# Performance work log

Measured on AMD Instinct MI355X. Metric: run time of the kernel, lower is better.

## Reference

```python
import jax, jax.numpy as jnp
import numpy as np

B, N, E = 32, 2048, 1048576  # 32 uniform graphs of 2048 nodes, avg degree 16
BN = B * N
KS = (1024, 512, 256)  # TopKPooling ratio=0.5 -> ceil(0.5*n) per layer (uniform graphs -> static)


def _mlp2(x, w1, b1, w2, b2):
    # nn.Sequential(Linear, ReLU, Linear)
    return jnp.maximum(x @ w1 + b1, 0.0) @ w2 + b2


def _forward(x, edge_attr, node_w1, node_b1, node_w2, node_b2,
             edge_w1, edge_b1, edge_w2, edge_b2,
             eff_in_w, eff_in_b, eff_h_w, eff_h_b, eff_out_w, eff_out_b,
             upd_in_w, upd_in_b, upd_h_w, upd_h_b, upd_out_w, upd_out_b,
             pool_w, edge_index):
    relu = lambda t: jnp.maximum(t, 0.0)
    src, dst = edge_index[0], edge_index[1]  # PyG: x_j = h[src], x_i = h[dst], aggregate at dst
    h = _mlp2(x, node_w1, node_b1, node_w2, node_b2)          # [BN, F] node embedding
    e = _mlp2(edge_attr, edge_w1, edge_b1, edge_w2, edge_b2)  # [E, F]  edge embedding
    node_mask = jnp.ones((BN,), bool)
    edge_mask = jnp.ones((E,), bool)
    for i in range(3):
        # --- DPIGNNLayer: gather-concat-MLP(+edge_attr) message, scatter-mean aggregate ---
        m = jnp.concatenate([h[dst], h[src]], axis=-1)        # [E, 2F] = cat(x_i, x_j)
        m = relu(m @ eff_in_w[i] + eff_in_b[i])
        m = relu(m @ eff_h_w[i] + eff_h_b[i])
        m = relu(m @ eff_out_w[i] + eff_out_b[i] + e)
        em = edge_mask.astype(h.dtype)[:, None]
        agg = jax.ops.segment_sum(m * em, dst, num_segments=BN)
        cnt = jax.ops.segment_sum(em, dst, num_segments=BN)
        mean = agg / jnp.maximum(cnt, 1.0)                    # mean aggr (0 where no edges)
        u = jnp.concatenate([mean, h], axis=-1)
        u = relu(u @ upd_in_w[i] + upd_in_b[i])
        u = relu(u @ upd_h_w[i] + upd_h_b[i])
        _ = relu(u @ upd_out_w[i] + upd_out_b[i] + h)  # dead compute: source update() returns x
        # --- TopKPooling(ratio=0.5), masked form (uniform graph sizes -> static k) ---
        w = pool_w[i]
        score = jnp.tanh((h @ w) / jnp.linalg.norm(w))        # [BN]
        masked = jnp.where(node_mask, score, -jnp.inf).reshape(B, N)
        _, idx = jax.lax.top_k(masked, KS[i])                 # [B, k]
        sel = jnp.zeros((B, N), bool).at[jnp.arange(B)[:, None], idx].set(True).reshape(-1)
        node_mask = sel
        h = jnp.where(node_mask[:, None], h * score[:, None], 0.0)
        edge_mask = edge_mask & node_mask[src] & node_mask[dst]  # filter_adj equivalent
    # global_mean_pool over surviving nodes per graph
    nm = node_mask.astype(h.dtype)[:, None]
    sums = (h * nm).reshape(B, N, -1).sum(axis=1)
    cnts = nm.reshape(B, N, 1).sum(axis=1)
    return sums / jnp.maximum(cnts, 1.0)  # [B, F]


def setup_inputs() -> dict:
    key = jax.random.key(0)
    ks = iter(jax.random.split(key, 40))
    F, ND, ED = 128, 16, 8
    s = 0.05
    W = lambda shape: jax.random.normal(next(ks), shape, jnp.float32) * s
    zb = lambda shape: jnp.zeros(shape, jnp.float32)
    e_per = E // B
    base = (jnp.arange(E) // e_per) * N  # graph offset per edge
    src = jax.random.randint(next(ks), (E,), 0, N) + base
    dst = jax.random.randint(next(ks), (E,), 0, N) + base
    return {
        'x': jax.random.normal(next(ks), (BN, ND), jnp.float32),
        'edge_attr': jax.random.normal(next(ks), (E, ED), jnp.float32),
        'node_w1': W((ND, F)), 'node_b1': zb((F,)),
        'node_w2': W((F, F)), 'node_b2': zb((F,)),
        'edge_w1': W((ED, F)), 'edge_b1': zb((F,)),
        'edge_w2': W((F, F)), 'edge_b2': zb((F,)),
        'eff_in_w': W((3, 2 * F, F)), 'eff_in_b': zb((3, F)),
        'eff_h_w': W((3, F, F)), 'eff_h_b': zb((3, F)),
        'eff_out_w': W((3, F, F)), 'eff_out_b': zb((3, F)),
        'upd_in_w': W((3, 2 * F, F)), 'upd_in_b': zb((3, F)),
        'upd_h_w': W((3, F, F)), 'upd_h_b': zb((3, F)),
        'upd_out_w': W((3, F, F)), 'upd_out_b': zb((3, F)),
        'pool_w': W((3, F)),
        'edge_index': jnp.stack([src, dst]),
    }


def reference(x, edge_attr, node_w1, node_b1, node_w2, node_b2,
              edge_w1, edge_b1, edge_w2, edge_b2,
              eff_in_w, eff_in_b, eff_h_w, eff_h_b, eff_out_w, eff_out_b,
              upd_in_w, upd_in_b, upd_h_w, upd_h_b, upd_out_w, upd_out_b,
              pool_w, edge_index):
    return _forward(x, edge_attr, node_w1, node_b1, node_w2, node_b2,
                    edge_w1, edge_b1, edge_w2, edge_b2,
                    eff_in_w, eff_in_b, eff_h_w, eff_h_b, eff_out_w, eff_out_b,
                    upd_in_w, upd_in_b, upd_h_w, upd_h_b, upd_out_w, upd_out_b,
                    pool_w, edge_index)
```

## Files before the change

### kernel.cpp

```cpp
#include <hip/hip_runtime.h>
#include <hip/hip_bf16.h>


#define NPG    2048
#define NGRAPH 32
#define HP     2112
#define HPAD(b) ((b) + ((b) >> 5))

__device__ __forceinline__ unsigned int mono_bits(float z) {
    unsigned int bb = __float_as_uint(z);
    return (bb & 0x80000000u) ? ~bb : (bb | 0x80000000u);
}
__device__ __forceinline__ float mono_decode(unsigned int mo) {
    unsigned int bb = (mo & 0x80000000u) ? (mo & 0x7FFFFFFFu) : ~mo;
    return __uint_as_float(bb);
}

__global__ __launch_bounds__(256) void k1_fused(
    const float* __restrict__ x,
    const float* __restrict__ W1,
    const float* __restrict__ b1,
    const float* __restrict__ W2,
    const float* __restrict__ b2,
    const float* __restrict__ pw,
    float4* __restrict__ d4)
{
    __shared__ __align__(16) float swn[384];
    __shared__ __align__(16) float sv[384];
    __shared__ float sc[4];
    __shared__ float snorm[3];
    int t = threadIdx.x;
    int lane = t & 63, wv = t >> 6;

    if (wv < 3) {
        float w0 = pw[wv * 128 + lane];
        float w1 = pw[wv * 128 + 64 + lane];
        float p = w0 * w0 + w1 * w1;
        #pragma unroll
        for (int s = 32; s; s >>= 1) p += __shfl_xor(p, s);
        if (lane == 0) snorm[wv] = sqrtf(p);
    }
    __syncthreads();
    for (int i = t; i < 384; i += 256) swn[i] = pw[i] / snorm[i >> 7];
    __syncthreads();
    for (int task = t; task < 387; task += 256) {
        int k = task / 129, j = task % 129;
        const float4* r4 = (const float4*)((j < 128) ? (W2 + j * 128) : b2);
        const float* wn = swn + k * 128;
        float p0 = 0.f, p1 = 0.f, p2 = 0.f, p3 = 0.f;
        #pragma unroll 8
        for (int q = 0; q < 32; ++q) {
            float4 w = r4[q];
            p0 = fmaf(w.x, wn[4 * q + 0], p0);
            p1 = fmaf(w.y, wn[4 * q + 1], p1);
            p2 = fmaf(w.z, wn[4 * q + 2], p2);
            p3 = fmaf(w.w, wn[4 * q + 3], p3);
        }
        float p = (p0 + p1) + (p2 + p3);
        if (j < 128) sv[k * 128 + j] = p;
        else sc[k] = p;
    }
    __syncthreads();

    const float4* W1v = (const float4*)W1;
    const float4* b1v = (const float4*)b1;
    int n = blockIdx.x * 256 + t;
    const float4* xr = (const float4*)(x + (size_t)n * 16);
    float4 xa = xr[0], xb = xr[1], xc = xr[2], xd = xr[3];
    float xs[16] = {xa.x, xa.y, xa.z, xa.w, xb.x, xb.y, xb.z, xb.w,
                    xc.x, xc.y, xc.z, xc.w, xd.x, xd.y, xd.z, xd.w};
    const float4* sv4 = (const float4*)sv;
    float dd0 = sc[0], dd1 = sc[1], dd2 = sc[2];
    #pragma unroll 4
    for (int fq = 0; fq < 32; ++fq) {
        float4 a4 = b1v[fq];
        #pragma unroll
        for (int j = 0; j < 16; ++j) {
            float4 w = W1v[j * 32 + fq];
            a4.x = fmaf(xs[j], w.x, a4.x);
            a4.y = fmaf(xs[j], w.y, a4.y);
            a4.z = fmaf(xs[j], w.z, a4.z);
            a4.w = fmaf(xs[j], w.w, a4.w);
        }
        a4.x = fmaxf(a4.x, 0.f); a4.y = fmaxf(a4.y, 0.f);
        a4.z = fmaxf(a4.z, 0.f); a4.w = fmaxf(a4.w, 0.f);
        float4 v0 = sv4[fq], v1 = sv4[32 + fq], v2 = sv4[64 + fq];
        dd0 = fmaf(a4.x, v0.x, fmaf(a4.y, v0.y, fmaf(a4.z, v0.z, fmaf(a4.w, v0.w, dd0))));
        dd1 = fmaf(a4.x, v1.x, fmaf(a4.y, v1.y, fmaf(a4.z, v1.z, fmaf(a4.w, v1.w, dd1))));
        dd2 = fmaf(a4.x, v2.x, fmaf(a4.y, v2.y, fmaf(a4.z, v2.z, fmaf(a4.w, v2.w, dd2))));
    }
    d4[n] = make_float4(dd0, dd1, dd2, 0.f);
}

__global__ __launch_bounds__(1024, 1) void k2_cascade(
    const float* __restrict__ x,
    const float* __restrict__ W1,
    const float* __restrict__ b1,
    const float* __restrict__ W2,
    const float* __restrict__ b2,
    const float4* __restrict__ d4,
    float* __restrict__ out)
{
    __shared__ unsigned long long sKey[NPG];
    __shared__ float d1A[NPG], d2A[NPG];
    __shared__ unsigned int hist[2][HP];
    __shared__ int   idxB[1024];
    __shared__ float cscB[1024], d1B[1024], d2B[1024];
    __shared__ int   idxA2[512];
    __shared__ float cscA2[512], d2A2[512];
    __shared__ float sW1[2048], sb1[128];
    __shared__ float Spart[1024], Svec[128], red4[4];
    __shared__ unsigned long long sPrefix;
    __shared__ int sNeed, sDone, sCnt;

    int t = threadIdx.x, g = blockIdx.x;
    int lane = t & 63, wv = t >> 6;
    const float4* d4g = d4 + (size_t)g * NPG;

    float4 e0 = d4g[t];
    float4 e1 = d4g[t + 1024];
    for (int i = t; i < 2048; i += 1024) sW1[i] = W1[i];
    if (t < 128) sb1[t] = b1[t];
    for (int i = t; i < 2 * HP; i += 1024) ((unsigned int*)hist)[i] = 0u;
    if (t == 0) { sPrefix = 0ull; sNeed = 1024; sDone = 0; sCnt = 0; }
    __syncthreads();

    {
        unsigned long long kv0 = ((unsigned long long)mono_bits(e0.x) << 11)
                               | (unsigned long long)(unsigned int)(2047 - t);
        d1A[t] = e0.y; d2A[t] = e0.z;
        sKey[t] = kv0;
        atomicAdd(&hist[0][HPAD((unsigned int)(kv0 >> 33) & 2047u)], 1u);
        int n1 = t + 1024;
        unsigned long long kv1 = ((unsigned long long)mono_bits(e1.x) << 11)
                               | (unsigned long long)(unsigned int)(2047 - n1);
        d1A[n1] = e1.y; d2A[n1] = e1.z;
        sKey[n1] = kv1;
        atomicAdd(&hist[0][HPAD((unsigned int)(kv1 >> 33) & 2047u)], 1u);
    }
    __syncthreads();

    int curN = NPG;
    for (int r = 0; r < 3; ++r) {
        int kk = 1024 >> r;
        const float* cscIn = (r == 1) ? cscB : cscA2;
        int*   idxOut = (r == 1) ? idxA2 : idxB;
        float* cscOut = (r == 1) ? cscA2 : cscB;

        if (r > 0) {
            const float* dIn   = (r == 1) ? d1B : d2A2;
            const int*   idxIn = (r == 1) ? idxB : idxA2;
            if (t == 0) { sPrefix = 0ull; sNeed = kk; sDone = 0; sCnt = 0; }
            __syncthreads();
            for (int m = t; m < curN; m += 1024) {
                float z = cscIn[m] * dIn[m];
                unsigned long long kv = ((unsigned long long)mono_bits(z) << 11)
                    | (unsigned long long)(unsigned int)(2047 - idxIn[m]);
                sKey[m] = kv;
                atomicAdd(&hist[0][HPAD((unsigned int)(kv >> 33) & 2047u)], 1u);
            }
            __syncthreads();
        }

        int lastBuf = 0;
        for (int pass = 0; pass < 4; ++pass) {
            int buf = pass & 1;
            int shift = 33 - 11 * pass;
            lastBuf = buf;
            if (pass > 0) {
                unsigned long long pref = sPrefix;
                for (int m = t; m < curN; m += 1024) {
                    unsigned long long kv = sKey[m];
                    if ((kv >> (shift + 11)) == (pref >> (shift + 11)))
                        atomicAdd(&hist[buf][HPAD((unsigned int)(kv >> shift) & 2047u)], 1u);
                }
                __syncthreads();
            }
            if (wv == 0) {
                unsigned long long pref = sPrefix;
                unsigned int need = (unsigned int)sNeed;
                unsigned int h[32], tl = 0;
                #pragma unroll
                for (int b = 0; b < 32; ++b) {
                    h[b] = hist[buf][HPAD(32u * t + b)];
                    tl += h[b];
                }
                unsigned int s = tl;
                #pragma unroll
                for (int d = 1; d < 64; d <<= 1) {
                    unsigned int v = __shfl_down(s, d);
                    if (t + d < 64) s += v;
                }
                unsigned int above = s - tl;
                if (above < need && above + tl >= need) {
                    unsigned int cum = above;
                    #pragma unroll
                    for (int b = 31; b >= 0; --b) {
                        cum += h[b];
                        if (cum >= need) {
                            int nn = (int)(need - (cum - h[b]));
                            sNeed = nn;
                            sPrefix = pref |
                                ((unsigned long long)(unsigned int)(32 * t + b) << shift);
                            sDone = (nn == (int)h[b]) || (pass == 3);
                            break;
                        }
                    }
                }
            } else if (pass > 0) {
                for (int i = t - 64; i < HP; i += 960) hist[buf ^ 1][i] = 0u;
            }
            __syncthreads();
            if (sDone) break;
        }
        unsigned long long thr = sPrefix;

        for (int i = t; i < HP; i += 1024) hist[lastBuf][i] = 0u;
        for (int m = t; m < curN; m += 1024) {
            unsigned long long kv = sKey[m];
            bool pred = (kv >= thr);
            unsigned long long mask = __ballot(pred);
            if (mask) {
                int leader = __ffsll((long long)mask) - 1;
                int cnt = __popcll(mask);
                int base = 0;
                if (lane == leader) base = atomicAdd(&sCnt, cnt);
                base = __shfl(base, leader);
                if (pred) {
                    int rank = __popcll(mask & ((1ull << lane) - 1ull));
                    int pos = base + rank;
                    float z = mono_decode((unsigned int)(kv >> 11));
                    int ni = 2047 - (int)((unsigned int)kv & 2047u);
                    idxOut[pos] = ni;
                    if (r == 0) {
                        cscOut[pos] = tanhf(z);
                        d1B[pos] = d1A[m]; d2B[pos] = d2A[m];
                    } else {
                        cscOut[pos] = cscIn[m] * tanhf(z);
                        if (r == 1) d2A2[pos] = d2B[m];
                    }
                }
            }
        }
        __syncthreads();
        curN = kk;
    }

    {
        int f = t & 127, grp = t >> 7;
        float Sacc = 0.f;
        #pragma unroll 2
        for (int it = grp; it < 256; it += 8) {
            int n = idxB[it];
            float cn = cscB[it];
            const float4* xr = (const float4*)(x + (size_t)(g * NPG + n) * 16);
            float4 xa = xr[0], xb = xr[1], xc = xr[2], xd = xr[3];
            float acc = sb1[f];
            acc = fmaf(xa.x, sW1[0 * 128 + f], acc);
            acc = fmaf(xa.y, sW1[1 * 128 + f], acc);
            acc = fmaf(xa.z, sW1[2 * 128 + f], acc);
            acc = fmaf(xa.w, sW1[3 * 128 + f], acc);
            acc = fmaf(xb.x, sW1[4 * 128 + f], acc);
            acc = fmaf(xb.y, sW1[5 * 128 + f], acc);
            acc = fmaf(xb.z, sW1[6 * 128 + f], acc);
            acc = fmaf(xb.w, sW1[7 * 128 + f], acc);
            acc = fmaf(xc.x, sW1[8 * 128 + f], acc);
            acc = fmaf(xc.y, sW1[9 * 128 + f], acc);
            acc = fmaf(xc.z, sW1[10 * 128 + f], acc);
            acc = fmaf(xc.w, sW1[11 * 128 + f], acc);
            acc = fmaf(xd.x, sW1[12 * 128 + f], acc);
            acc = fmaf(xd.y, sW1[13 * 128 + f], acc);
            acc = fmaf(xd.z, sW1[14 * 128 + f], acc);
            acc = fmaf(xd.w, sW1[15 * 128 + f], acc);
            Sacc += fmaxf(acc, 0.f) * cn;
        }
        Spart[t] = Sacc;
    }
    if (t < 256) {
        float cpart = cscB[t];
        #pragma unroll
        for (int s = 32; s; s >>= 1) cpart += __shfl_xor(cpart, s);
        if ((t & 63) == 0) red4[t >> 6] = cpart;
    }
    __syncthreads();
    if (t < 128) {
        float sv = 0.f;
        #pragma unroll
        for (int h = 0; h < 8; ++h) sv += Spart[h * 128 + t];
        Svec[t] = sv;
    }
    __syncthreads();
    {
        int f = t & 127, jc = t >> 7;
        float part = 0.f;
        #pragma unroll
        for (int j = 16 * jc; j < 16 * jc + 16; ++j)
            part = fmaf(Svec[j], W2[j * 128 + f], part);
        Spart[t] = part;
    }
    __syncthreads();
    if (t < 128) {
        float Csum = (red4[0] + red4[1]) + (red4[2] + red4[3]);
        float acc = Csum * b2[t];
        #pragma unroll
        for (int h = 0; h < 8; ++h) acc += Spart[h * 128 + t];
        out[g * 128 + t] = acc * (1.0f / 256.0f);
    }
}

extern "C" void kernel_launch(void* const* d_in, const int* in_sizes, int n_in,
                              void* d_out, int out_size, void* d_ws, size_t ws_size,
                              hipStream_t stream) {
    const float* x  = (const float*)d_in[0];
    const float* W1 = (const float*)d_in[2];
    const float* b1 = (const float*)d_in[3];
    const float* W2 = (const float*)d_in[4];
    const float* b2 = (const float*)d_in[5];
    const float* pw = (const float*)d_in[22];
    float* out = (float*)d_out;

    float4* d4 = (float4*)d_ws;

    k1_fused<<<256, 256, 0, stream>>>(x, W1, b1, W2, b2, pw, d4);
    k2_cascade<<<NGRAPH, 1024, 0, stream>>>(x, W1, b1, W2, b2, d4, out);
}
```

Baseline: 175.6 us.

## Stage W1 in LDS, two nodes per thread, register-resident top-k keys

The first kernel now copies W1 and b1 into shared memory and has each thread process two nodes, so it launches half as many blocks and reuses each weight load. The cascade kernel drops the shared key and score arrays and keeps each node's radix-select key in registers, with each pooling round unrolled as its own block. Selected x rows are gathered into shared memory once before the final readout instead of each thread group reloading them from global memory. The risks are higher register pressure and fewer blocks in kernel one, which may leave much of the GPU idle.

```diff
diff --git a/kernel.cpp b/kernel.cpp
--- a/kernel.cpp
+++ b/kernel.cpp
@@ -25,6 +25,8 @@
     const float* __restrict__ pw,
     float4* __restrict__ d4)
 {
+    __shared__ float4 sW1v[512];
+    __shared__ float4 sb1v[32];
     __shared__ __align__(16) float swn[384];
     __shared__ __align__(16) float sv[384];
     __shared__ float sc[4];
@@ -32,6 +34,8 @@
     int t = threadIdx.x;
     int lane = t & 63, wv = t >> 6;
 
+    for (int i = t; i < 512; i += 256) sW1v[i] = ((const float4*)W1)[i];
+    if (t < 32) sb1v[t] = ((const float4*)b1)[t];
     if (wv < 3) {
         float w0 = pw[wv * 128 + lane];
         float w1 = pw[wv * 128 + 64 + lane];
@@ -62,34 +66,49 @@
     }
     __syncthreads();
 
-    const float4* W1v = (const float4*)W1;
-    const float4* b1v = (const float4*)b1;
-    int n = blockIdx.x * 256 + t;
-    const float4* xr = (const float4*)(x + (size_t)n * 16);
-    float4 xa = xr[0], xb = xr[1], xc = xr[2], xd = xr[3];
+    int n0 = blockIdx.x * 512 + t;
+    int n1 = n0 + 256;
+    const float4* xr0 = (const float4*)(x + (size_t)n0 * 16);
+    const float4* xr1 = (const float4*)(x + (size_t)n1 * 16);
+    float4 xa = xr0[0], xb = xr0[1], xc = xr0[2], xd = xr0[3];
+    float4 ya = xr1[0], yb = xr1[1], yc = xr1[2], yd = xr1[3];
     float xs[16] = {xa.x, xa.y, xa.z, xa.w, xb.x, xb.y, xb.z, xb.w,
                     xc.x, xc.y, xc.z, xc.w, xd.x, xd.y, xd.z, xd.w};
+    float ys[16] = {ya.x, ya.y, ya.z, ya.w, yb.x, yb.y, yb.z, yb.w,
+                    yc.x, yc.y, yc.z, yc.w, yd.x, yd.y, yd.z, yd.w};
     const float4* sv4 = (const float4*)sv;
-    float dd0 = sc[0], dd1 = sc[1], dd2 = sc[2];
+    float d00 = sc[0], d01 = sc[1], d02 = sc[2];
+    float d10 = sc[0], d11 = sc[1], d12 = sc[2];
     #pragma unroll 4
     for (int fq = 0; fq < 32; ++fq) {
-        float4 a4 = b1v[fq];
+        float4 bb = sb1v[fq];
+        float4 a4 = bb, c4 = bb;
         #pragma unroll
         for (int j = 0; j < 16; ++j) {
-            float4 w = W1v[j * 32 + fq];
+            float4 w = sW1v[j * 32 + fq];
             a4.x = fmaf(xs[j], w.x, a4.x);
             a4.y = fmaf(xs[j], w.y, a4.y);
             a4.z = fmaf(xs[j], w.z, a4.z);
             a4.w = fmaf(xs[j], w.w, a4.w);
+            c4.x = fmaf(ys[j], w.x, c4.x);
+            c4.y = fmaf(ys[j], w.y, c4.y);
+            c4.z = fmaf(ys[j], w.z, c4.z);
+            c4.w = fmaf(ys[j], w.w, c4.w);
         }
         a4.x = fmaxf(a4.x, 0.f); a4.y = fmaxf(a4.y, 0.f);
         a4.z = fmaxf(a4.z, 0.f); a4.w = fmaxf(a4.w, 0.f);
+        c4.x = fmaxf(c4.x, 0.f); c4.y = fmaxf(c4.y, 0.f);
+        c4.z = fmaxf(c4.z, 0.f); c4.w = fmaxf(c4.w, 0.f);
         float4 v0 = sv4[fq], v1 = sv4[32 + fq], v2 = sv4[64 + fq];
-        dd0 = fmaf(a4.x, v0.x, fmaf(a4.y, v0.y, fmaf(a4.z, v0.z, fmaf(a4.w, v0.w, dd0))));
-        dd1 = fmaf(a4.x, v1.x, fmaf(a4.y, v1.y, fmaf(a4.z, v1.z, fmaf(a4.w, v1.w, dd1))));
-        dd2 = fmaf(a4.x, v2.x, fmaf(a4.y, v2.y, fmaf(a4.z, v2.z, fmaf(a4.w, v2.w, dd2))));
-    }
-    d4[n] = make_float4(dd0, dd1, dd2, 0.f);
+        d00 = fmaf(a4.x, v0.x, fmaf(a4.y, v0.y, fmaf(a4.z, v0.z, fmaf(a4.w, v0.w, d00))));
+        d01 = fmaf(a4.x, v1.x, fmaf(a4.y, v1.y, fmaf(a4.z, v1.z, fmaf(a4.w, v1.w, d01))));
+        d02 = fmaf(a4.x, v2.x, fmaf(a4.y, v2.y, fmaf(a4.z, v2.z, fmaf(a4.w, v2.w, d02))));
+        d10 = fmaf(c4.x, v0.x, fmaf(c4.y, v0.y, fmaf(c4.z, v0.z, fmaf(c4.w, v0.w, d10))));
+        d11 = fmaf(c4.x, v1.x, fmaf(c4.y, v1.y, fmaf(c4.z, v1.z, fmaf(c4.w, v1.w, d11))));
+        d12 = fmaf(c4.x, v2.x, fmaf(c4.y, v2.y, fmaf(c4.z, v2.z, fmaf(c4.w, v2.w, d12))));
+    }
+    d4[n0] = make_float4(d00, d01, d02, 0.f);
+    d4[n1] = make_float4(d10, d11, d12, 0.f);
 }
 
 __global__ __launch_bounds__(1024, 1) void k2_cascade(
@@ -101,14 +120,13 @@
     const float4* __restrict__ d4,
     float* __restrict__ out)
 {
-    __shared__ unsigned long long sKey[NPG];
-    __shared__ float d1A[NPG], d2A[NPG];
     __shared__ unsigned int hist[2][HP];
     __shared__ int   idxB[1024];
     __shared__ float cscB[1024], d1B[1024], d2B[1024];
     __shared__ int   idxA2[512];
     __shared__ float cscA2[512], d2A2[512];
     __shared__ float sW1[2048], sb1[128];
+    __shared__ float4 xg[256][4];
     __shared__ float Spart[1024], Svec[128], red4[4];
     __shared__ unsigned long long sPrefix;
     __shared__ int sNeed, sDone, sCnt;
@@ -125,43 +143,50 @@
     if (t == 0) { sPrefix = 0ull; sNeed = 1024; sDone = 0; sCnt = 0; }
     __syncthreads();
 
-    {
-        unsigned long long kv0 = ((unsigned long long)mono_bits(e0.x) << 11)
-                               | (unsigned long long)(unsigned int)(2047 - t);
-        d1A[t] = e0.y; d2A[t] = e0.z;
-        sKey[t] = kv0;
-        atomicAdd(&hist[0][HPAD((unsigned int)(kv0 >> 33) & 2047u)], 1u);
-        int n1 = t + 1024;
-        unsigned long long kv1 = ((unsigned long long)mono_bits(e1.x) << 11)
-                               | (unsigned long long)(unsigned int)(2047 - n1);
-        d1A[n1] = e1.y; d2A[n1] = e1.z;
-        sKey[n1] = kv1;
-        atomicAdd(&hist[0][HPAD((unsigned int)(kv1 >> 33) & 2047u)], 1u);
-    }
-    __syncthreads();
-
-    int curN = NPG;
-    for (int r = 0; r < 3; ++r) {
-        int kk = 1024 >> r;
-        const float* cscIn = (r == 1) ? cscB : cscA2;
-        int*   idxOut = (r == 1) ? idxA2 : idxB;
-        float* cscOut = (r == 1) ? cscA2 : cscB;
-
-        if (r > 0) {
-            const float* dIn   = (r == 1) ? d1B : d2A2;
-            const int*   idxIn = (r == 1) ? idxB : idxA2;
-            if (t == 0) { sPrefix = 0ull; sNeed = kk; sDone = 0; sCnt = 0; }
-            __syncthreads();
-            for (int m = t; m < curN; m += 1024) {
-                float z = cscIn[m] * dIn[m];
-                unsigned long long kv = ((unsigned long long)mono_bits(z) << 11)
-                    | (unsigned long long)(unsigned int)(2047 - idxIn[m]);
-                sKey[m] = kv;
-                atomicAdd(&hist[0][HPAD((unsigned int)(kv >> 33) & 2047u)], 1u);
-            }
-            __syncthreads();
-        }
-
+    unsigned long long kv0 = ((unsigned long long)mono_bits(e0.x) << 11)
+                           | (unsigned long long)(unsigned int)(2047 - t);
+    unsigned long long kv1 = ((unsigned long long)mono_bits(e1.x) << 11)
+                           | (unsigned long long)(unsigned int)(1023 - t);
+    atomicAdd(&hist[0][HPAD((unsigned int)(kv0 >> 33) & 2047u)], 1u);
+    atomicAdd(&hist[0][HPAD((unsigned int)(kv1 >> 33) & 2047u)], 1u);
+    __syncthreads();
+
+    auto scan_pass = [&](int buf, int shift, int pass) {
+        if (wv == 0) {
+            unsigned long long pref = sPrefix;
+            unsigned int need = (unsigned int)sNeed;
+            unsigned int h[32], tl = 0;
+            #pragma unroll
+            for (int b = 0; b < 32; ++b) {
+                h[b] = hist[buf][HPAD(32u * t + b)];
+                tl += h[b];
+            }
+            unsigned int s = tl;
+            #pragma unroll
+            for (int d = 1; d < 64; d <<= 1) {
+                unsigned int v = __shfl_down(s, d);
+                if (t + d < 64) s += v;
+            }
+            unsigned int above = s - tl;
+            if (above < need && above + tl >= need) {
+                unsigned int cum = above;
+                #pragma unroll
+                for (int b = 31; b >= 0; --b) {
+                    cum += h[b];
+                    if (cum >= need) {
+                        int nn = (int)(need - (cum - h[b]));
+                        sNeed = nn;
+                        sPrefix = pref |
+                            ((unsigned long long)(unsigned int)(32 * t + b) << shift);
+                        sDone = (nn == (int)h[b]) || (pass == 3);
+                        break;
+                    }
+                }
+            }
+        }
+    };
+
+    {
         int lastBuf = 0;
         for (int pass = 0; pass < 4; ++pass) {
             int buf = pass & 1;
@@ -169,92 +194,156 @@
             lastBuf = buf;
             if (pass > 0) {
                 unsigned long long pref = sPrefix;
-                for (int m = t; m < curN; m += 1024) {
-                    unsigned long long kv = sKey[m];
-                    if ((kv >> (shift + 11)) == (pref >> (shift + 11)))
-                        atomicAdd(&hist[buf][HPAD((unsigned int)(kv >> shift) & 2047u)], 1u);
-                }
+                if ((kv0 >> (shift + 11)) == (pref >> (shift + 11)))
+                    atomicAdd(&hist[buf][HPAD((unsigned int)(kv0 >> shift) & 2047u)], 1u);
+                if ((kv1 >> (shift + 11)) == (pref >> (shift + 11)))
+                    atomicAdd(&hist[buf][HPAD((unsigned int)(kv1 >> shift) & 2047u)], 1u);
                 __syncthreads();
             }
-            if (wv == 0) {
-                unsigned long long pref = sPrefix;
-                unsigned int need = (unsigned int)sNeed;
-                unsigned int h[32], tl = 0;
-                #pragma unroll
-                for (int b = 0; b < 32; ++b) {
-                    h[b] = hist[buf][HPAD(32u * t + b)];
-                    tl += h[b];
-                }
-                unsigned int s = tl;
-                #pragma unroll
-                for (int d = 1; d < 64; d <<= 1) {
-                    unsigned int v = __shfl_down(s, d);
-                    if (t + d < 64) s += v;
-                }
-                unsigned int above = s - tl;
-                if (above < need && above + tl >= need) {
-                    unsigned int cum = above;
-                    #pragma unroll
-                    for (int b = 31; b >= 0; --b) {
-                        cum += h[b];
-                        if (cum >= need) {
-                            int nn = (int)(need - (cum - h[b]));
-                            sNeed = nn;
-                            sPrefix = pref |
-                                ((unsigned long long)(unsigned int)(32 * t + b) << shift);
-                            sDone = (nn == (int)h[b]) || (pass == 3);
-                            break;
-                        }
-                    }
-                }
-            } else if (pass > 0) {
+            scan_pass(buf, shift, pass);
+            if (wv != 0 && pass > 0)
                 for (int i = t - 64; i < HP; i += 960) hist[buf ^ 1][i] = 0u;
-            }
             __syncthreads();
             if (sDone) break;
         }
         unsigned long long thr = sPrefix;
-
         for (int i = t; i < HP; i += 1024) hist[lastBuf][i] = 0u;
-        for (int m = t; m < curN; m += 1024) {
-            unsigned long long kv = sKey[m];
+        #pragma unroll
+        for (int half = 0; half < 2; ++half) {
+            unsigned long long kv = half ? kv1 : kv0;
+            float dy = half ? e1.y : e0.y;
+            float dz = half ? e1.z : e0.z;
             bool pred = (kv >= thr);
             unsigned long long mask = __ballot(pred);
             if (mask) {
                 int leader = __ffsll((long long)mask) - 1;
-                int cnt = __popcll(mask);
                 int base = 0;
-                if (lane == leader) base = atomicAdd(&sCnt, cnt);
+                if (lane == leader) base = atomicAdd(&sCnt, __popcll(mask));
                 base = __shfl(base, leader);
                 if (pred) {
-                    int rank = __popcll(mask & ((1ull << lane) - 1ull));
-                    int pos = base + rank;
+                    int pos = base + __popcll(mask & ((1ull << lane) - 1ull));
                     float z = mono_decode((unsigned int)(kv >> 11));
-                    int ni = 2047 - (int)((unsigned int)kv & 2047u);
-                    idxOut[pos] = ni;
-                    if (r == 0) {
-                        cscOut[pos] = tanhf(z);
-                        d1B[pos] = d1A[m]; d2B[pos] = d2A[m];
-                    } else {
-                        cscOut[pos] = cscIn[m] * tanhf(z);
-                        if (r == 1) d2A2[pos] = d2B[m];
-                    }
+                    idxB[pos] = 2047 - (int)((unsigned int)kv & 2047u);
+                    cscB[pos] = tanhf(z);
+                    d1B[pos] = dy; d2B[pos] = dz;
                 }
             }
         }
         __syncthreads();
-        curN = kk;
-    }
-
+    }
+
+    {
+        if (t == 0) { sPrefix = 0ull; sNeed = 512; sDone = 0; sCnt = 0; }
+        float ci = cscB[t], dv = d1B[t], d2r = d2B[t];
+        int ni = idxB[t];
+        float z = ci * dv;
+        unsigned long long kv = ((unsigned long long)mono_bits(z) << 11)
+                              | (unsigned long long)(unsigned int)(2047 - ni);
+        __syncthreads();
+        atomicAdd(&hist[0][HPAD((unsigned int)(kv >> 33) & 2047u)], 1u);
+        __syncthreads();
+        int lastBuf = 0;
+        for (int pass = 0; pass < 4; ++pass) {
+            int buf = pass & 1;
+            int shift = 33 - 11 * pass;
+            lastBuf = buf;
+            if (pass > 0) {
+                unsigned long long pref = sPrefix;
+                if ((kv >> (shift + 11)) == (pref >> (shift + 11)))
+                    atomicAdd(&hist[buf][HPAD((unsigned int)(kv >> shift) & 2047u)], 1u);
+                __syncthreads();
+            }
+            scan_pass(buf, shift, pass);
+            if (wv != 0 && pass > 0)
+                for (int i = t - 64; i < HP; i += 960) hist[buf ^ 1][i] = 0u;
+            __syncthreads();
+            if (sDone) break;
+        }
+        unsigned long long thr = sPrefix;
+        for (int i = t; i < HP; i += 1024) hist[lastBuf][i] = 0u;
+        bool pred = (kv >= thr);
+        unsigned long long mask = __ballot(pred);
+        if (mask) {
+            int leader = __ffsll((long long)mask) - 1;
+            int base = 0;
+            if (lane == leader) base = atomicAdd(&sCnt, __popcll(mask));
+            base = __shfl(base, leader);
+            if (pred) {
+                int pos = base + __popcll(mask & ((1ull << lane) - 1ull));
+                float zz = mono_decode((unsigned int)(kv >> 11));
+                idxA2[pos] = ni;
+                cscA2[pos] = ci * tanhf(zz);
+                d2A2[pos] = d2r;
+            }
+        }
+        __syncthreads();
+    }
+
+    {
+        if (t == 0) { sPrefix = 0ull; sNeed = 256; sDone = 0; sCnt = 0; }
+        float ci = 0.f; int ni = 0;
+        unsigned long long kv = 0ull;
+        if (t < 512) {
+            ci = cscA2[t]; ni = idxA2[t];
+            float z = ci * d2A2[t];
+            kv = ((unsigned long long)mono_bits(z) << 11)
+               | (unsigned long long)(unsigned int)(2047 - ni);
+        }
+        __syncthreads();
+        if (t < 512)
+            atomicAdd(&hist[0][HPAD((unsigned int)(kv >> 33) & 2047u)], 1u);
+        __syncthreads();
+        int lastBuf = 0;
+        for (int pass = 0; pass < 4; ++pass) {
+            int buf = pass & 1;
+            int shift = 33 - 11 * pass;
+            lastBuf = buf;
+            if (pass > 0) {
+                unsigned long long pref = sPrefix;
+                if (t < 512 &&
+                    (kv >> (shift + 11)) == (pref >> (shift + 11)))
+                    atomicAdd(&hist[buf][HPAD((unsigned int)(kv >> shift) & 2047u)], 1u);
+                __syncthreads();
+            }
+            scan_pass(buf, shift, pass);
+            if (wv != 0 && pass > 0)
+                for (int i = t - 64; i < HP; i += 960) hist[buf ^ 1][i] = 0u;
+            __syncthreads();
+            if (sDone) break;
+        }
+        unsigned long long thr = sPrefix;
+        if (t < 512) {
+            bool pred = (kv >= thr);
+            unsigned long long mask = __ballot(pred);
+            if (mask) {
+                int leader = __ffsll((long long)mask) - 1;
+                int base = 0;
+                if (lane == leader) base = atomicAdd(&sCnt, __popcll(mask));
+                base = __shfl(base, leader);
+                if (pred) {
+                    int pos = base + __popcll(mask & ((1ull << lane) - 1ull));
+                    float zz = mono_decode((unsigned int)(kv >> 11));
+                    idxB[pos] = ni;
+                    cscB[pos] = ci * tanhf(zz);
+                }
+            }
+        }
+        __syncthreads();
+    }
+
+    {
+        int i = t >> 2, j = t & 3;
+        const float4* xr = (const float4*)(x + (size_t)(g * NPG + idxB[i]) * 16);
+        xg[i][j] = xr[j];
+    }
+    __syncthreads();
     {
         int f = t & 127, grp = t >> 7;
         float Sacc = 0.f;
         #pragma unroll 2
         for (int it = grp; it < 256; it += 8) {
-            int n = idxB[it];
             float cn = cscB[it];
-            const float4* xr = (const float4*)(x + (size_t)(g * NPG + n) * 16);
-            float4 xa = xr[0], xb = xr[1], xc = xr[2], xd = xr[3];
+            float4 xa = xg[it][0], xb = xg[it][1], xc = xg[it][2], xd = xg[it][3];
             float acc = sb1[f];
             acc = fmaf(xa.x, sW1[0 * 128 + f], acc);
             acc = fmaf(xa.y, sW1[1 * 128 + f], acc);
@@ -321,6 +410,6 @@
 
     float4* d4 = (float4*)d_ws;
 
-    k1_fused<<<256, 256, 0, stream>>>(x, W1, b1, W2, b2, pw, d4);
+    k1_fused<<<128, 256, 0, stream>>>(x, W1, b1, W2, b2, pw, d4);
     k2_cascade<<<NGRAPH, 1024, 0, stream>>>(x, W1, b1, W2, b2, d4, out);
 }
```

Measured after the change: 176.3 us. No clear change (+0.4%).
